# Kernel optimization log

Measured on AMD Instinct MI355X. Metric: run time of the kernel, lower is better.

The kernel has to match this reference:

```python
import jax, jax.numpy as jnp
import numpy as np
from jax import lax


def setup_inputs() -> dict:
    key = jax.random.key(0)
    k1, k2 = jax.random.split(key)
    B, T, D, O = 8, 8192, 512, 512
    x = jax.random.normal(k1, (B, T, D), dtype=jnp.float32)
    # Dense kernel over concat([h_t, state]) -> width 2*D
    W = jax.random.normal(k2, (2 * D, O), dtype=jnp.float32) * (1.0 / np.sqrt(2 * D))
    b = jnp.zeros((O,), dtype=jnp.float32)
    decay = jnp.float32(0.95)
    return {"x": x, "W": W, "b": b, "decay": decay}


def reference(x, W, b, decay):
    # x: [B, T, D]; W: [2D, O]; b: [O]; decay: scalar lambda
    B, T, D = x.shape
    lam = jnp.clip(decay, 0.5, 0.999)  # keras constraint on the decay weight
    h_avg = jnp.mean(x, axis=0)  # [T, D] batch-mean per timestep

    # EMA recurrence: s_t = lam * s_{t-1} + (1 - lam) * h_avg_t, s_{-1} = 0
    def step(s, a):
        s = lam * s + (1.0 - lam) * a
        return s, s

    _, states = lax.scan(step, jnp.zeros((D,), x.dtype), h_avg)  # [T, D]

    # proj(concat([h_t, s_t])) = h_t @ W_h + s_t @ W_s + b (fused, no concat materialized)
    W_h, W_s = W[:D], W[D:]
    out = jnp.einsum('btd,do->bto', x, W_h) + jnp.einsum('td,do->to', states, W_s)[None] + b
    return out  # [B, T, O]
```

## Files before the change

kernel.cpp:

```cpp
#include <hip/hip_runtime.h>
#include <hip/hip_bf16.h>
#include <stdint.h>

#define T_DIM 8192
#define B_DIM 8
#define D_DIM 512
#define O_DIM 512

typedef __attribute__((ext_vector_type(4))) float f32x4;
typedef __attribute__((ext_vector_type(8))) short short8;
typedef __attribute__((ext_vector_type(4))) unsigned short us4;

__device__ __forceinline__ unsigned short f2bf(float f) {
  union { float f; uint32_t u; } v; v.f = f;
  uint32_t u = v.u + 0x7FFFu + ((v.u >> 16) & 1u);
  return (unsigned short)(u >> 16);
}

__device__ __forceinline__ uint32_t cvtpk(float a, float b) {
  uint32_t r;
  asm("v_cvt_pk_bf16_f32 %0, %1, %2" : "=v"(r) : "v"(a), "v"(b));
  return r;
}

__device__ __forceinline__ void gload_lds16(const void* g, void* l) {
  __builtin_amdgcn_global_load_lds(
      (const __attribute__((address_space(1))) void*)g,
      (__attribute__((address_space(3))) void*)l, 16, 0, 0);
}

__device__ __forceinline__ float clip_lam(const float* decay) {
  return fminf(fmaxf(decay[0], 0.5f), 0.999f);
}

__global__ void mean_cvt_kernel(const float* __restrict__ x, float* __restrict__ havg,
                                unsigned short* __restrict__ xbf) {
  int idx = blockIdx.x * 256 + threadIdx.x;
  const f32x4* x4 = (const f32x4*)x;
  us4* xb4 = (us4*)xbf;
  const size_t stride = (size_t)T_DIM * D_DIM / 4;
  f32x4 s = {0.f, 0.f, 0.f, 0.f};
#pragma unroll
  for (int b = 0; b < B_DIM; ++b) {
    f32x4 v = x4[(size_t)b * stride + idx];
    s += v;
    us4 o;
#pragma unroll
    for (int j = 0; j < 4; ++j) o[j] = f2bf(v[j]);
    xb4[(size_t)b * stride + idx] = o;
  }
  s *= 0.125f;
  ((f32x4*)havg)[idx] = s;
}

__global__ void mean_kernel(const float* __restrict__ x, float* __restrict__ havg) {
  int idx = blockIdx.x * 256 + threadIdx.x;
  const f32x4* x4 = (const f32x4*)x;
  const size_t stride = (size_t)T_DIM * D_DIM / 4;
  f32x4 s = {0.f, 0.f, 0.f, 0.f};
#pragma unroll
  for (int b = 0; b < B_DIM; ++b) s += x4[(size_t)b * stride + idx];
  s *= 0.125f;
  ((f32x4*)havg)[idx] = s;
}

__global__ void wconv_kernel(const float* __restrict__ W, unsigned short* __restrict__ Wt) {
  __shared__ float tile[64][65];
  int bk = blockIdx.x >> 3;
  int bn = blockIdx.x & 7;
  int tr = threadIdx.x >> 4;
  int tc = threadIdx.x & 15;
#pragma unroll
  for (int i = 0; i < 4; ++i) {
    int row = i * 16 + tr;
    f32x4 v = *(const f32x4*)&W[(size_t)(bk * 64 + row) * O_DIM + bn * 64 + tc * 4];
#pragma unroll
    for (int j = 0; j < 4; ++j) tile[row][tc * 4 + j] = v[j];
  }
  __syncthreads();
#pragma unroll
  for (int i = 0; i < 4; ++i) {
    int nl = i * 16 + tr;
    us4 o;
#pragma unroll
    for (int j = 0; j < 4; ++j) o[j] = f2bf(tile[tc * 4 + j][nl]);
    int kg = bk * 64 + tc * 4;
    int h = kg >> 9;
    int k = kg & 511;
    *(us4*)&Wt[(size_t)h * (512 * 512) + (size_t)(bn * 64 + nl) * 512 + k] = o;
  }
}

#define CHUNK 128
#define NCHUNK (T_DIM / CHUNK)

__global__ void scanA_kernel(float* __restrict__ havg, const float* __restrict__ decay) {
  int chunk = blockIdx.x >> 1;
  int d = ((blockIdx.x & 1) << 8) + threadIdx.x;
  float lam = clip_lam(decay);
  float om = 1.0f - lam;
  size_t base = (size_t)chunk * CHUNK * D_DIM + d;
  float cur[16], nxt[16];
#pragma unroll
  for (int i = 0; i < 16; ++i) cur[i] = havg[base + (size_t)i * D_DIM];
  float s = 0.f;
  for (int blk = 0; blk < 8; ++blk) {
    if (blk < 7) {
#pragma unroll
      for (int i = 0; i < 16; ++i)
        nxt[i] = havg[base + (size_t)((blk + 1) * 16 + i) * D_DIM];
    }
#pragma unroll
    for (int i = 0; i < 16; ++i) {
      s = lam * s + om * cur[i];
      havg[base + (size_t)(blk * 16 + i) * D_DIM] = s;
    }
#pragma unroll
    for (int i = 0; i < 16; ++i) cur[i] = nxt[i];
  }
}

__global__ void scanB_kernel(const float* __restrict__ havg, const float* __restrict__ decay,
                             float* __restrict__ carry) {
  int d = blockIdx.x * 256 + threadIdx.x;
  float lam = clip_lam(decay);
  float l2 = lam * lam;
  float l4 = l2 * l2;
  float l8 = l4 * l4;
  float l16 = l8 * l8;
  float l32 = l16 * l16;
  float l64 = l32 * l32;
  float l128 = l64 * l64;
  float e[NCHUNK];
#pragma unroll
  for (int c = 0; c < NCHUNK; ++c)
    e[c] = havg[((size_t)c * CHUNK + CHUNK - 1) * D_DIM + d];
  float s = 0.f;
#pragma unroll
  for (int c = 0; c < NCHUNK; ++c) {
    s = l128 * s + e[c];
    carry[c * D_DIM + d] = s;
  }
}

__global__ void scanC_kernel(const float* __restrict__ havg, const float* __restrict__ carry,
                             const float* __restrict__ decay, unsigned short* __restrict__ st) {
  int idx = blockIdx.x * 256 + threadIdx.x;
  int t = idx >> 7;
  int d4 = idx & 127;
  int c = t >> 7;
  int k = t & 127;
  float lam = clip_lam(decay);
  float w = exp2f((float)(k + 1) * __log2f(lam));
  f32x4 p = ((const f32x4*)havg)[idx];
  f32x4 cin = {0.f, 0.f, 0.f, 0.f};
  if (c > 0) cin = ((const f32x4*)carry)[(size_t)(c - 1) * 128 + d4];
  us4 o;
#pragma unroll
  for (int j = 0; j < 4; ++j) o[j] = f2bf(p[j] + w * cin[j]);
  ((us4*)st)[idx] = o;
}

template <bool ADD_SBAR>
__global__ __launch_bounds__(256, 2)
void gemm128bf(const unsigned short* __restrict__ A, const unsigned short* __restrict__ Bt,
               const float* __restrict__ extra, float* __restrict__ C) {
  __shared__ __align__(16) char smem[16384];
  unsigned short* Bs = (unsigned short*)(smem + 8192);

  int nwg = gridDim.x;
  int bid = blockIdx.x;
  int swz = (bid & 7) * (nwg >> 3) + (bid >> 3);
  int tm = swz >> 2, tn = swz & 3;
  int brow = tm << 7, bcol = tn << 7;

  int tid = threadIdx.x;
  int wave = tid >> 6, lane = tid & 63;
  int wr = (wave >> 1) << 6, wc = (wave & 1) << 6;
  const int lr = lane & 15, lkb = lane >> 4;

  const int srow = lane >> 2;
  const int soct = ((lane & 3) ^ ((lane >> 3) & 3)) << 3;
  const int pm = (lr >> 1) & 3;

  f32x4 acc[4][4];
#pragma unroll
  for (int m = 0; m < 4; ++m)
#pragma unroll
    for (int n = 0; n < 4; ++n) acc[m][n] = (f32x4){0.f, 0.f, 0.f, 0.f};

  for (int kt = 0; kt < 512 / 32; ++kt) {
    int k0 = kt << 5;
#pragma unroll
    for (int it = 0; it < 2; ++it) {
      int q = (it << 2) + wave;
      int row = (q << 4) + srow;
      gload_lds16(A + (size_t)(brow + row) * 512 + k0 + soct, smem + (q << 10));
      gload_lds16(Bt + (size_t)(bcol + row) * 512 + k0 + soct, (char*)Bs + (q << 10));
    }
    __syncthreads();

    const unsigned short* As = (const unsigned short*)smem;
    short8 af[4], bfr[4];
#pragma unroll
    for (int m = 0; m < 4; ++m)
      af[m] = *(const short8*)(As + (size_t)(wr + (m << 4) + lr) * 32 + ((lkb ^ pm) << 3));
#pragma unroll
    for (int n = 0; n < 4; ++n)
      bfr[n] = *(const short8*)(Bs + (size_t)(wc + (n << 4) + lr) * 32 + ((lkb ^ pm) << 3));

#pragma unroll
    for (int m = 0; m < 4; ++m)
#pragma unroll
      for (int n = 0; n < 4; ++n)
        acc[m][n] = __builtin_amdgcn_mfma_f32_16x16x32_bf16(af[m], bfr[n], acc[m][n], 0, 0, 0);
    __syncthreads();
  }

#pragma unroll
  for (int m = 0; m < 4; ++m) {
    int row0 = brow + wr + (m << 4) + ((lane >> 4) << 2);
#pragma unroll
    for (int n = 0; n < 4; ++n) {
      int col = bcol + wc + (n << 4) + lr;
#pragma unroll
      for (int j = 0; j < 4; ++j) {
        int row = row0 + j;
        float v = acc[m][n][j];
        if constexpr (ADD_SBAR)
          v += extra[(size_t)(row & (T_DIM - 1)) * O_DIM + col];
        else
          v += extra[col];
        C[(size_t)row * O_DIM + col] = v;
      }
    }
  }
}

__global__ __launch_bounds__(256, 2)
void gemm128f32(const float* __restrict__ Ag, const unsigned short* __restrict__ Bt,
                const float* __restrict__ extra, float* __restrict__ C) {
  __shared__ __align__(16) char smem[16384 + 8192];
  unsigned short* Bs = (unsigned short*)(smem + 16384);

  int nwg = gridDim.x;
  int bid = blockIdx.x;
  int swz = (bid & 7) * (nwg >> 3) + (bid >> 3);
  int tm = swz >> 2, tn = swz & 3;
  int brow = tm << 7, bcol = tn << 7;

  int tid = threadIdx.x;
  int wave = tid >> 6, lane = tid & 63;
  int wr = (wave >> 1) << 6, wc = (wave & 1) << 6;
  const int lr = lane & 15, lkb = lane >> 4;

  f32x4 acc[4][4];
#pragma unroll
  for (int m = 0; m < 4; ++m)
#pragma unroll
    for (int n = 0; n < 4; ++n) acc[m][n] = (f32x4){0.f, 0.f, 0.f, 0.f};

  for (int kt = 0; kt < 512 / 32; ++kt) {
    int k0 = kt << 5;
#pragma unroll
    for (int it = 0; it < 4; ++it) {
      int q = (it << 2) + wave;
      int row = (q << 3) + (lane >> 3);
      int kc = ((lane & 7) ^ (lane >> 3)) << 2;
      gload_lds16(Ag + (size_t)(brow + row) * 512 + k0 + kc, smem + (q << 10));
    }
#pragma unroll
    for (int it = 0; it < 2; ++it) {
      int q = (it << 2) + wave;
      int n = (q << 4) + (lane >> 2);
      int kc = (lane & 3) << 3;
      gload_lds16(Bt + (size_t)(bcol + n) * 512 + k0 + kc, (char*)Bs + (q << 10));
    }
    __syncthreads();

    short8 af[4], bfr[4];
    const float* As = (const float*)smem;
#pragma unroll
    for (int m = 0; m < 4; ++m) {
      int row = wr + (m << 4) + lr;
      int r7 = row & 7;
      int b0 = lkb << 1;
      f32x4 lo = *(const f32x4*)(As + row * 32 + ((b0 ^ r7) << 2));
      f32x4 hi = *(const f32x4*)(As + row * 32 + (((b0 + 1) ^ r7) << 2));
      union { short8 s; uint32_t u[4]; } t;
      t.u[0] = cvtpk(lo[0], lo[1]); t.u[1] = cvtpk(lo[2], lo[3]);
      t.u[2] = cvtpk(hi[0], hi[1]); t.u[3] = cvtpk(hi[2], hi[3]);
      af[m] = t.s;
    }
#pragma unroll
    for (int n = 0; n < 4; ++n)
      bfr[n] = *(const short8*)(Bs + (size_t)(wc + (n << 4) + lr) * 32 + (lkb << 3));

#pragma unroll
    for (int m = 0; m < 4; ++m)
#pragma unroll
      for (int n = 0; n < 4; ++n)
        acc[m][n] = __builtin_amdgcn_mfma_f32_16x16x32_bf16(af[m], bfr[n], acc[m][n], 0, 0, 0);
    __syncthreads();
  }

#pragma unroll
  for (int m = 0; m < 4; ++m) {
    int row0 = brow + wr + (m << 4) + ((lane >> 4) << 2);
#pragma unroll
    for (int n = 0; n < 4; ++n) {
      int col = bcol + wc + (n << 4) + lr;
#pragma unroll
      for (int j = 0; j < 4; ++j) {
        int row = row0 + j;
        C[(size_t)row * O_DIM + col] =
            acc[m][n][j] + extra[(size_t)(row & (T_DIM - 1)) * O_DIM + col];
      }
    }
  }
}

extern "C" void kernel_launch(void* const* d_in, const int* in_sizes, int n_in,
                              void* d_out, int out_size, void* d_ws, size_t ws_size,
                              hipStream_t stream) {
  (void)in_sizes; (void)n_in; (void)out_size;
  const float* x     = (const float*)d_in[0];
  const float* W     = (const float*)d_in[1];
  const float* bias  = (const float*)d_in[2];
  const float* decay = (const float*)d_in[3];
  float* out = (float*)d_out;

  char* ws = (char*)d_ws;
  size_t off = 0;
  float*          havg  = (float*)(ws + off);          off += 16777216;
  unsigned short* st    = (unsigned short*)(ws + off); off += 8388608;
  unsigned short* Wt    = (unsigned short*)(ws + off); off += 1048576;
  float*          sbar  = (float*)(ws + off);          off += 16777216;
  float*          carry = (float*)(ws + off);          off += 131072;
  unsigned short* xbf   = (unsigned short*)(ws + off); off += (size_t)B_DIM * T_DIM * D_DIM * 2;
  const bool use_bf = (ws_size >= off);

  if (use_bf) {
    mean_cvt_kernel<<<T_DIM * D_DIM / 4 / 256, 256, 0, stream>>>(x, havg, xbf);
  } else {
    mean_kernel<<<T_DIM * D_DIM / 4 / 256, 256, 0, stream>>>(x, havg);
  }
  wconv_kernel<<<128, 256, 0, stream>>>(W, Wt);
  scanA_kernel<<<NCHUNK * 2, 256, 0, stream>>>(havg, decay);
  scanB_kernel<<<2, 256, 0, stream>>>(havg, decay, carry);
  scanC_kernel<<<T_DIM * D_DIM / 4 / 256, 256, 0, stream>>>(havg, carry, decay, st);
  gemm128bf<false><<<(T_DIM / 128) * 4, 256, 0, stream>>>(st, Wt + 512 * 512, bias, sbar);
  if (use_bf) {
    gemm128bf<true><<<(B_DIM * T_DIM / 128) * 4, 256, 0, stream>>>(xbf, Wt, sbar, out);
  } else {
    gemm128f32<<<(B_DIM * T_DIM / 128) * 4, 256, 0, stream>>>(x, Wt, sbar, out);
  }
}
```

Measured before the change: 145.5 us.

## Double-buffer LDS in bf16 GEMM and vectorize epilogue via LDS transpose

Splits shared memory into two stages so global-to-LDS loads for the next K tile are issued before computing the current one, removing one barrier per iteration. The epilogue now stages accumulators through LDS so each lane writes contiguous float4 rows, coalescing the output and bias/state reads. Launch bounds are raised to request more waves per CU, which may pressure registers given doubled LDS footprint.

```diff
diff --git a/kernel.cpp b/kernel.cpp
--- a/kernel.cpp
+++ b/kernel.cpp
@@ -162,11 +162,10 @@
 }
 
 template <bool ADD_SBAR>
-__global__ __launch_bounds__(256, 2)
+__global__ __launch_bounds__(256, 4)
 void gemm128bf(const unsigned short* __restrict__ A, const unsigned short* __restrict__ Bt,
                const float* __restrict__ extra, float* __restrict__ C) {
-  __shared__ __align__(16) char smem[16384];
-  unsigned short* Bs = (unsigned short*)(smem + 8192);
+  __shared__ __align__(16) char smem[2][16384];
 
   int nwg = gridDim.x;
   int bid = blockIdx.x;
@@ -189,18 +188,30 @@
 #pragma unroll
     for (int n = 0; n < 4; ++n) acc[m][n] = (f32x4){0.f, 0.f, 0.f, 0.f};
 
-  for (int kt = 0; kt < 512 / 32; ++kt) {
-    int k0 = kt << 5;
-#pragma unroll
-    for (int it = 0; it < 2; ++it) {
-      int q = (it << 2) + wave;
-      int row = (q << 4) + srow;
-      gload_lds16(A + (size_t)(brow + row) * 512 + k0 + soct, smem + (q << 10));
-      gload_lds16(Bt + (size_t)(bcol + row) * 512 + k0 + soct, (char*)Bs + (q << 10));
-    }
-    __syncthreads();
-
-    const unsigned short* As = (const unsigned short*)smem;
+  const size_t arow0 = (size_t)(brow + (wave << 4) + srow) * 512 + soct;
+  const size_t brow0 = (size_t)(bcol + (wave << 4) + srow) * 512 + soct;
+
+#define STAGE(buf, kt)                                                          \
+  {                                                                             \
+    int k0_ = (kt) << 5;                                                        \
+    _Pragma("unroll")                                                           \
+    for (int it = 0; it < 2; ++it) {                                            \
+      int q = (it << 2) + wave;                                                 \
+      gload_lds16(A + arow0 + (size_t)(it << 15) + k0_, &smem[buf][q << 10]);   \
+      gload_lds16(Bt + brow0 + (size_t)(it << 15) + k0_,                        \
+                  &smem[buf][8192 + (q << 10)]);                                \
+    }                                                                           \
+  }
+
+  STAGE(0, 0);
+  __syncthreads();
+
+  for (int kt = 0; kt < 16; ++kt) {
+    int cur = kt & 1;
+    if (kt < 15) STAGE(cur ^ 1, kt + 1);
+
+    const unsigned short* As = (const unsigned short*)&smem[cur][0];
+    const unsigned short* Bs = (const unsigned short*)&smem[cur][8192];
     short8 af[4], bfr[4];
 #pragma unroll
     for (int m = 0; m < 4; ++m)
@@ -214,26 +225,36 @@
 #pragma unroll
       for (int n = 0; n < 4; ++n)
         acc[m][n] = __builtin_amdgcn_mfma_f32_16x16x32_bf16(af[m], bfr[n], acc[m][n], 0, 0, 0);
-    __syncthreads();
-  }
-
+
+    __syncthreads();
+  }
+#undef STAGE
+
+  float* tp = (float*)&smem[0][0] + (size_t)wave * 2048;
 #pragma unroll
   for (int m = 0; m < 4; ++m) {
-    int row0 = brow + wr + (m << 4) + ((lane >> 4) << 2);
-#pragma unroll
-    for (int n = 0; n < 4; ++n) {
-      int col = bcol + wc + (n << 4) + lr;
-#pragma unroll
-      for (int j = 0; j < 4; ++j) {
-        int row = row0 + j;
-        float v = acc[m][n][j];
-        if constexpr (ADD_SBAR)
-          v += extra[(size_t)(row & (T_DIM - 1)) * O_DIM + col];
-        else
-          v += extra[col];
-        C[(size_t)row * O_DIM + col] = v;
-      }
-    }
+#pragma unroll
+    for (int n = 0; n < 4; ++n)
+#pragma unroll
+      for (int j = 0; j < 4; ++j)
+        tp[((lkb << 2) + j) * 68 + (n << 4) + lr] = acc[m][n][j];
+    __syncthreads();
+#pragma unroll
+    for (int p = 0; p < 4; ++p) {
+      int rl = (p << 2) + (lane >> 4);
+      int c0 = (lane & 15) << 2;
+      f32x4 v = *(const f32x4*)(tp + rl * 68 + c0);
+      int row = brow + wr + (m << 4) + rl;
+      int col = bcol + wc + c0;
+      f32x4 e;
+      if constexpr (ADD_SBAR)
+        e = *(const f32x4*)&extra[(size_t)(row & (T_DIM - 1)) * O_DIM + col];
+      else
+        e = *(const f32x4*)&extra[col];
+      v += e;
+      *(f32x4*)&C[(size_t)row * O_DIM + col] = v;
+    }
+    __syncthreads();
   }
 }
 
```

After: 143.3 us. Within noise of the previous version (-1.5%).
